# Kernel optimization log

Hardware: AMD Instinct MI355X
Metric: run time of the kernel (lower is better)

## Reference

```python
import jax, jax.numpy as jnp
import numpy as np

VOCAB = 50000
D_EMB = 300
N_BINS = 11
B, LQ, LD = 64, 32, 1024
MU = np.array([1.0, 0.9, 0.7, 0.5, 0.3, 0.1, -0.1, -0.3, -0.5, -0.7, -0.9], dtype=np.float32)
SIGMA = np.array([1e-3] + [0.1] * 10, dtype=np.float32)


def setup_inputs() -> dict:
    key = jax.random.key(0)
    ks = jax.random.split(key, 8)
    inputs_q = jax.random.randint(ks[0], (B, LQ), 0, VOCAB, dtype=jnp.int64 if jax.config.jax_enable_x64 else jnp.int32)
    inputs_d = jax.random.randint(ks[1], (B, LD), 0, VOCAB, dtype=jnp.int64 if jax.config.jax_enable_x64 else jnp.int32)
    mask_q = jnp.ones((B, LQ), dtype=jnp.float32)
    mask_d = jnp.ones((B, LD), dtype=jnp.float32)
    word_emb = jax.random.normal(ks[2], (VOCAB, D_EMB), dtype=jnp.float32) * 0.1
    attn_table = jax.random.uniform(ks[3], (VOCAB, 1), dtype=jnp.float32)  # frozen IDF embedding
    idf_w = jax.random.normal(ks[4], (1, 1), dtype=jnp.float32)
    idf_b = jnp.zeros((1,), dtype=jnp.float32)
    dense_w = jax.random.normal(ks[5], (1, N_BINS), dtype=jnp.float32) * 0.1
    dense_b = jnp.zeros((1,), dtype=jnp.float32)
    return {
        'inputs_q': inputs_q, 'inputs_d': inputs_d,
        'mask_q': mask_q, 'mask_d': mask_d,
        'word_emb': word_emb, 'attn_table': attn_table,
        'idf_w': idf_w, 'idf_b': idf_b,
        'dense_w': dense_w, 'dense_b': dense_b,
    }


def _l2_normalize(x, eps=1e-12):
    # matches F.normalize(x, 2, dim=-1): x / max(||x||, eps)
    n = jnp.sqrt(jnp.sum(x * x, axis=-1, keepdims=True))
    return x / jnp.maximum(n, eps)


def reference(inputs_q, inputs_d, mask_q, mask_d, word_emb, attn_table,
              idf_w, idf_b, dense_w, dense_b):
    mu = jnp.asarray(MU)        # [K]
    sigma = jnp.asarray(SIGMA)  # [K]
    # idf attention on query tokens: Linear(1,1) on frozen embedding lookup
    attn_q = attn_table[inputs_q] * idf_w[0, 0] + idf_b[0]          # [B,Lq,1]
    q_embed = _l2_normalize(word_emb[inputs_q])                      # [B,Lq,E]
    d_embed = _l2_normalize(word_emb[inputs_d])                      # [B,Ld,E]
    sim = jnp.einsum('bqe,bde->bqd', q_embed, d_embed)               # [B,Lq,Ld]
    # RBF soft-histogram over n_bins kernels, doc tokens masked
    rbf = jnp.exp(-((sim[..., None] - mu) ** 2) / (sigma ** 2) / 2)  # [B,Lq,Ld,K]
    pooling_sum = jnp.einsum('bqdk,bd->bqk', rbf, mask_d)            # [B,Lq,K]
    wq = mask_q[..., None] * attn_q                                   # [B,Lq,1]
    log_pool = jnp.log(jnp.clip(pooling_sum, 1e-10)) * wq * 0.01     # [B,Lq,K]
    log_pooling_sum = jnp.sum(log_pool, axis=1)                      # [B,K]
    out = jnp.tanh(log_pooling_sum @ dense_w.T + dense_b)            # [B,1]
    return out[:, 0]                                                 # [B]
```

## Files before the change

### kernel.cpp

```cpp
#include <hip/hip_runtime.h>
#include <math.h>

#define VOCAB  50000
#define D_EMB  300
#define NBINS  11
#define BATCH  64
#define LQ     32
#define LD     1024
#define DTILE  64
#define NDT    (LD / DTILE)
#define NSTEP  10
#define FRAG_SHORTS (NSTEP * 512)

typedef __attribute__((ext_vector_type(8))) short short8;
typedef __attribute__((ext_vector_type(4))) float floatx4;

__constant__ float c_mu[NBINS]  = {1.0f, 0.9f, 0.7f, 0.5f, 0.3f, 0.1f,
                                   -0.1f, -0.3f, -0.5f, -0.7f, -0.9f};
__constant__ float c_is2[NBINS] = {500000.0f, 50.f, 50.f, 50.f, 50.f, 50.f,
                                   50.f, 50.f, 50.f, 50.f, 50.f};

static __device__ __forceinline__ unsigned short f32_bf16(float f) {
  unsigned u = __float_as_uint(f);
  u += 0x7FFFu + ((u >> 16) & 1u);
  return (unsigned short)(u >> 16);
}
static __device__ __forceinline__ float bf16_f32(unsigned short h) {
  return __uint_as_float(((unsigned)h) << 16);
}

static __device__ __forceinline__ float stage_rows(
    const float* __restrict__ emb_row,
    short* __restrict__ region, int khi, int lane)
{
  const float4* emb4 = (const float4*)emb_row;
  float p = 0.f;
#pragma unroll
  for (int s = 0; s < NSTEP; ++s) {
    const int k0 = 32 * s + 8 * khi;
    float4 fa = make_float4(0.f, 0.f, 0.f, 0.f);
    float4 fb = make_float4(0.f, 0.f, 0.f, 0.f);
    if (k0 < D_EMB)     fa = emb4[k0 >> 2];
    if (k0 + 4 < D_EMB) fb = emb4[(k0 >> 2) + 1];
    unsigned short h[8];
    h[0] = f32_bf16(fa.x); h[1] = f32_bf16(fa.y);
    h[2] = f32_bf16(fa.z); h[3] = f32_bf16(fa.w);
    h[4] = f32_bf16(fb.x); h[5] = f32_bf16(fb.y);
    h[6] = f32_bf16(fb.z); h[7] = f32_bf16(fb.w);
    short8 v;
#pragma unroll
    for (int j = 0; j < 8; ++j) {
      const float x = bf16_f32(h[j]);
      p += x * x;
      v[j] = (short)h[j];
    }
    *(short8*)(region + s * 512 + lane * 8) = v;
  }
  return p;
}

__global__ __launch_bounds__(256) void knrm_expand(
    const int* __restrict__ inputs_q, const int* __restrict__ inputs_d,
    const float* __restrict__ word_emb, short* __restrict__ afrag,
    short* __restrict__ dfrag, float* __restrict__ invq,
    float* __restrict__ invd)
{
  const int b    = blockIdx.y;
  const int i    = blockIdx.x * 4 + (threadIdx.x >> 6);
  const int lane = threadIdx.x & 63;
  const int khi  = lane >> 4, rl = lane & 15;
  if (i >= 66) return;

  int tok; short* dst;
  if (i < 2) {
    tok = inputs_q[b * LQ + i * 16 + rl];
    dst = afrag + (size_t)(b * 2 + i) * FRAG_SHORTS;
  } else {
    const int g = i - 2;
    tok = inputs_d[b * LD + g * 16 + rl];
    dst = dfrag + (size_t)(b * 64 + g) * FRAG_SHORTS;
  }
  float p = stage_rows(word_emb + (size_t)tok * D_EMB, dst, khi, lane);
  p += __shfl_xor(p, 16); p += __shfl_xor(p, 32);
  if (lane < 16) {
    const float inv = 1.f / fmaxf(sqrtf(p), 1e-12f);
    if (i < 2) invq[b * LQ + i * 16 + lane] = inv;
    else       invd[b * LD + (i - 2) * 16 + lane] = inv;
  }
}

__global__ __launch_bounds__(256) void knrm_main(
    const float* __restrict__ mask_d, const short* __restrict__ afrag,
    const short* __restrict__ dfrag, const float* __restrict__ invq,
    const float* __restrict__ invd, float* __restrict__ partial)
{
  const int b    = blockIdx.y;
  const int dt   = blockIdx.x;
  const int tid  = threadIdx.x;
  const int wid  = tid >> 6;
  const int lane = tid & 63;
  const int khi  = lane >> 4;
  const int rl   = lane & 15;
  const int qt   = wid >> 1;
  const int dp   = wid & 1;

  __shared__ float red[4][16][NBINS];

  const short8* arow = (const short8*)(afrag + (size_t)(b * 2 + qt) * FRAG_SHORTS);
  const short8* b0r  = (const short8*)(dfrag + (size_t)(b * 64 + dt * 4 + 2 * dp) * FRAG_SHORTS);
  const short8* b1r  = b0r + FRAG_SHORTS / 8;

  floatx4 acc0 = {0.f, 0.f, 0.f, 0.f};
  floatx4 acc1 = {0.f, 0.f, 0.f, 0.f};
#pragma unroll
  for (int s = 0; s < NSTEP; ++s) {
    const short8 a  = arow[s * 64 + lane];
    const short8 b0 = b0r [s * 64 + lane];
    const short8 b1 = b1r [s * 64 + lane];
    acc0 = __builtin_amdgcn_mfma_f32_16x16x32_bf16(a, b0, acc0, 0, 0, 0);
    acc1 = __builtin_amdgcn_mfma_f32_16x16x32_bf16(a, b1, acc1, 0, 0, 0);
  }

  const int dbase = b * LD + dt * DTILE;
  const float iq_own = invq[b * LQ + 16 * qt + rl];
  float iq[4];
#pragma unroll
  for (int r = 0; r < 4; ++r) iq[r] = __shfl(iq_own, 4 * khi + r);
  const float id0 = invd[dbase + 32 * dp + rl];
  const float id1 = invd[dbase + 32 * dp + 16 + rl];
  const float md0 = mask_d[dbase + 32 * dp + rl];
  const float md1 = mask_d[dbase + 32 * dp + 16 + rl];

  float ps[4][NBINS];
#pragma unroll
  for (int r = 0; r < 4; ++r) {
    const float s0 = acc0[r] * iq[r] * id0;
    const float s1 = acc1[r] * iq[r] * id1;
#pragma unroll
    for (int k = 0; k < NBINS; ++k) {
      const float d0 = s0 - c_mu[k];
      const float d1 = s1 - c_mu[k];
      ps[r][k] = md0 * __expf(-d0 * d0 * c_is2[k])
               + md1 * __expf(-d1 * d1 * c_is2[k]);
    }
  }

#pragma unroll
  for (int off = 1; off < 16; off <<= 1)
#pragma unroll
    for (int r = 0; r < 4; ++r)
#pragma unroll
      for (int k = 0; k < NBINS; ++k)
        ps[r][k] += __shfl_xor(ps[r][k], off);

  if (rl == 0)
#pragma unroll
    for (int r = 0; r < 4; ++r)
#pragma unroll
      for (int k = 0; k < NBINS; ++k)
        red[wid][4 * khi + r][k] = ps[r][k];
  __syncthreads();

  for (int v = tid; v < LQ * NBINS; v += 256) {
    const int q = v / NBINS, k = v % NBINS;
    const float sv = (q < 16) ? (red[0][q][k] + red[1][q][k])
                              : (red[2][q - 16][k] + red[3][q - 16][k]);
    partial[((size_t)(b * LQ + q) * NBINS + k) * NDT + dt] = sv;
  }
}

__global__ __launch_bounds__(128) void knrm_finalize(
    const float* __restrict__ partial, const int* __restrict__ inputs_q,
    const float* __restrict__ mask_q, const float* __restrict__ attn_table,
    const float* __restrict__ idf_w, const float* __restrict__ idf_b,
    const float* __restrict__ dense_w, const float* __restrict__ dense_b,
    float* __restrict__ out)
{
  const int b   = blockIdx.x;
  const int tid = threadIdx.x;
  __shared__ float pool[LQ][NBINS];
  __shared__ float wq_s[LQ];
  __shared__ float lps[NBINS];

  for (int v = tid; v < LQ * NBINS; v += 128) {
    const int q = v / NBINS, k = v % NBINS;
    const float* p = partial + ((size_t)(b * LQ + q) * NBINS + k) * NDT;
    float s = 0.f;
#pragma unroll
    for (int t = 0; t < NDT; ++t) s += p[t];
    pool[q][k] = logf(fmaxf(s, 1e-10f));
  }
  if (tid < LQ) {
    const int tok = inputs_q[b * LQ + tid];
    wq_s[tid] = mask_q[b * LQ + tid] * (attn_table[tok] * idf_w[0] + idf_b[0]);
  }
  __syncthreads();
  if (tid < NBINS) {
    float s = 0.f;
    for (int q = 0; q < LQ; ++q) s += pool[q][tid] * wq_s[q];
    lps[tid] = 0.01f * s;
  }
  __syncthreads();
  if (tid == 0) {
    float z = dense_b[0];
    for (int k = 0; k < NBINS; ++k) z += lps[k] * dense_w[k];
    out[b] = tanhf(z);
  }
}

extern "C" void kernel_launch(void* const* d_in, const int* in_sizes, int n_in,
                              void* d_out, int out_size, void* d_ws, size_t ws_size,
                              hipStream_t stream) {
  const int*   inputs_q  = (const int*)d_in[0];
  const int*   inputs_d  = (const int*)d_in[1];
  const float* mask_q    = (const float*)d_in[2];
  const float* mask_d    = (const float*)d_in[3];
  const float* word_emb  = (const float*)d_in[4];
  const float* attn_tab  = (const float*)d_in[5];
  const float* idf_w     = (const float*)d_in[6];
  const float* idf_b     = (const float*)d_in[7];
  const float* dense_w   = (const float*)d_in[8];
  const float* dense_b   = (const float*)d_in[9];
  float* out = (float*)d_out;

  char*  ws      = (char*)d_ws;
  float* partial = (float*)ws;
  short* afrag   = (short*)(ws + (2u  << 20));
  short* dfrag   = (short*)(ws + (4u  << 20));
  float* invq    = (float*)(ws + (48u << 20));
  float* invd    = (float*)(ws + (49u << 20));

  dim3 egrid(17, BATCH);
  knrm_expand<<<egrid, 256, 0, stream>>>(inputs_q, inputs_d, word_emb,
                                         afrag, dfrag, invq, invd);
  dim3 grid(NDT, BATCH);
  knrm_main<<<grid, 256, 0, stream>>>(mask_d, afrag, dfrag, invq, invd, partial);
  knrm_finalize<<<BATCH, 128, 0, stream>>>(partial, inputs_q, mask_q, attn_tab,
                                           idf_w, idf_b, dense_w, dense_b, out);
}
```

Before: 146.5 us.

## Fuse embedding gather and bf16 conversion into the MFMA similarity kernel

Merges the expand kernel into the main kernel. Each block gathers its own doc-token embeddings straight into register fragments and stages the query fragments in LDS. This removes the global round trip of bf16 fragments and inverse norms, plus one kernel launch. Each block now covers 128 doc tokens with both query tiles per wave, giving 8 chunks per batch, so the grid shrinks to 512 blocks. The query embeddings are gathered again by every chunk block, and the larger register-resident fragments may lower occupancy.

```diff
diff --git a/kernel.cpp b/kernel.cpp
--- a/kernel.cpp
+++ b/kernel.cpp
@@ -1,15 +1,14 @@
 #include <hip/hip_runtime.h>
 #include <math.h>
 
-#define VOCAB  50000
-#define D_EMB  300
-#define NBINS  11
-#define BATCH  64
-#define LQ     32
-#define LD     1024
-#define DTILE  64
-#define NDT    (LD / DTILE)
-#define NSTEP  10
+#define VOCAB   50000
+#define D_EMB   300
+#define NBINS   11
+#define BATCH   64
+#define LQ      32
+#define LD      1024
+#define NCHUNK  8
+#define NSTEP   10
 #define FRAG_SHORTS (NSTEP * 512)
 
 typedef __attribute__((ext_vector_type(8))) short short8;
@@ -29,9 +28,9 @@
   return __uint_as_float(((unsigned)h) << 16);
 }
 
-static __device__ __forceinline__ float stage_rows(
-    const float* __restrict__ emb_row,
-    short* __restrict__ region, int khi, int lane)
+static __device__ __forceinline__ float gather_convert(
+    const float* __restrict__ emb_row, short8* __restrict__ frag,
+    int khi)
 {
   const float4* emb4 = (const float4*)emb_row;
   float p = 0.f;
@@ -54,118 +53,104 @@
       p += x * x;
       v[j] = (short)h[j];
     }
-    *(short8*)(region + s * 512 + lane * 8) = v;
+    frag[s] = v;
   }
   return p;
 }
 
-__global__ __launch_bounds__(256) void knrm_expand(
+__global__ __launch_bounds__(256, 2) void knrm_fused(
     const int* __restrict__ inputs_q, const int* __restrict__ inputs_d,
-    const float* __restrict__ word_emb, short* __restrict__ afrag,
-    short* __restrict__ dfrag, float* __restrict__ invq,
-    float* __restrict__ invd)
+    const float* __restrict__ mask_d, const float* __restrict__ word_emb,
+    float* __restrict__ partial)
 {
   const int b    = blockIdx.y;
-  const int i    = blockIdx.x * 4 + (threadIdx.x >> 6);
-  const int lane = threadIdx.x & 63;
-  const int khi  = lane >> 4, rl = lane & 15;
-  if (i >= 66) return;
-
-  int tok; short* dst;
-  if (i < 2) {
-    tok = inputs_q[b * LQ + i * 16 + rl];
-    dst = afrag + (size_t)(b * 2 + i) * FRAG_SHORTS;
-  } else {
-    const int g = i - 2;
-    tok = inputs_d[b * LD + g * 16 + rl];
-    dst = dfrag + (size_t)(b * 64 + g) * FRAG_SHORTS;
-  }
-  float p = stage_rows(word_emb + (size_t)tok * D_EMB, dst, khi, lane);
-  p += __shfl_xor(p, 16); p += __shfl_xor(p, 32);
-  if (lane < 16) {
-    const float inv = 1.f / fmaxf(sqrtf(p), 1e-12f);
-    if (i < 2) invq[b * LQ + i * 16 + lane] = inv;
-    else       invd[b * LD + (i - 2) * 16 + lane] = inv;
-  }
-}
-
-__global__ __launch_bounds__(256) void knrm_main(
-    const float* __restrict__ mask_d, const short* __restrict__ afrag,
-    const short* __restrict__ dfrag, const float* __restrict__ invq,
-    const float* __restrict__ invd, float* __restrict__ partial)
-{
-  const int b    = blockIdx.y;
-  const int dt   = blockIdx.x;
+  const int j    = blockIdx.x;
   const int tid  = threadIdx.x;
   const int wid  = tid >> 6;
   const int lane = tid & 63;
   const int khi  = lane >> 4;
   const int rl   = lane & 15;
-  const int qt   = wid >> 1;
-  const int dp   = wid & 1;
-
-  __shared__ float red[4][16][NBINS];
-
-  const short8* arow = (const short8*)(afrag + (size_t)(b * 2 + qt) * FRAG_SHORTS);
-  const short8* b0r  = (const short8*)(dfrag + (size_t)(b * 64 + dt * 4 + 2 * dp) * FRAG_SHORTS);
-  const short8* b1r  = b0r + FRAG_SHORTS / 8;
-
-  floatx4 acc0 = {0.f, 0.f, 0.f, 0.f};
-  floatx4 acc1 = {0.f, 0.f, 0.f, 0.f};
+
+  __shared__ __align__(16) short Alds[2 * FRAG_SHORTS];
+  __shared__ float invq_lds[LQ];
+  __shared__ float red[4][2][16][NBINS];
+
+  const int dbase = b * LD + j * 128 + 32 * wid;
+
+  const int td0 = inputs_d[dbase + rl];
+  const int td1 = inputs_d[dbase + 16 + rl];
+  short8 bf0[NSTEP], bf1[NSTEP];
+  float pb0 = gather_convert(word_emb + (size_t)td0 * D_EMB, bf0, khi);
+  float pb1 = gather_convert(word_emb + (size_t)td1 * D_EMB, bf1, khi);
+  pb0 += __shfl_xor(pb0, 16); pb0 += __shfl_xor(pb0, 32);
+  pb1 += __shfl_xor(pb1, 16); pb1 += __shfl_xor(pb1, 32);
+  const float id0 = 1.f / fmaxf(sqrtf(pb0), 1e-12f);
+  const float id1 = 1.f / fmaxf(sqrtf(pb1), 1e-12f);
+
+  if (wid < 2) {
+    const int tq = inputs_q[b * LQ + 16 * wid + rl];
+    short8 af[NSTEP];
+    float pa = gather_convert(word_emb + (size_t)tq * D_EMB, af, khi);
+    short8* dst = (short8*)(Alds + wid * FRAG_SHORTS);
+#pragma unroll
+    for (int s = 0; s < NSTEP; ++s) dst[s * 64 + lane] = af[s];
+    pa += __shfl_xor(pa, 16); pa += __shfl_xor(pa, 32);
+    if (lane < 16) invq_lds[16 * wid + lane] = 1.f / fmaxf(sqrtf(pa), 1e-12f);
+  }
+  __syncthreads();
+
+  floatx4 acc[2][2] = {{{0.f,0.f,0.f,0.f},{0.f,0.f,0.f,0.f}},
+                       {{0.f,0.f,0.f,0.f},{0.f,0.f,0.f,0.f}}};
 #pragma unroll
   for (int s = 0; s < NSTEP; ++s) {
-    const short8 a  = arow[s * 64 + lane];
-    const short8 b0 = b0r [s * 64 + lane];
-    const short8 b1 = b1r [s * 64 + lane];
-    acc0 = __builtin_amdgcn_mfma_f32_16x16x32_bf16(a, b0, acc0, 0, 0, 0);
-    acc1 = __builtin_amdgcn_mfma_f32_16x16x32_bf16(a, b1, acc1, 0, 0, 0);
-  }
-
-  const int dbase = b * LD + dt * DTILE;
-  const float iq_own = invq[b * LQ + 16 * qt + rl];
-  float iq[4];
-#pragma unroll
-  for (int r = 0; r < 4; ++r) iq[r] = __shfl(iq_own, 4 * khi + r);
-  const float id0 = invd[dbase + 32 * dp + rl];
-  const float id1 = invd[dbase + 32 * dp + 16 + rl];
-  const float md0 = mask_d[dbase + 32 * dp + rl];
-  const float md1 = mask_d[dbase + 32 * dp + 16 + rl];
-
-  float ps[4][NBINS];
-#pragma unroll
-  for (int r = 0; r < 4; ++r) {
-    const float s0 = acc0[r] * iq[r] * id0;
-    const float s1 = acc1[r] * iq[r] * id1;
-#pragma unroll
-    for (int k = 0; k < NBINS; ++k) {
-      const float d0 = s0 - c_mu[k];
-      const float d1 = s1 - c_mu[k];
-      ps[r][k] = md0 * __expf(-d0 * d0 * c_is2[k])
-               + md1 * __expf(-d1 * d1 * c_is2[k]);
+    const short8 a0 = *(const short8*)(Alds + s * 512 + lane * 8);
+    const short8 a1 = *(const short8*)(Alds + FRAG_SHORTS + s * 512 + lane * 8);
+    acc[0][0] = __builtin_amdgcn_mfma_f32_16x16x32_bf16(a0, bf0[s], acc[0][0], 0, 0, 0);
+    acc[0][1] = __builtin_amdgcn_mfma_f32_16x16x32_bf16(a0, bf1[s], acc[0][1], 0, 0, 0);
+    acc[1][0] = __builtin_amdgcn_mfma_f32_16x16x32_bf16(a1, bf0[s], acc[1][0], 0, 0, 0);
+    acc[1][1] = __builtin_amdgcn_mfma_f32_16x16x32_bf16(a1, bf1[s], acc[1][1], 0, 0, 0);
+  }
+
+  const float md0 = mask_d[dbase + rl];
+  const float md1 = mask_d[dbase + 16 + rl];
+#pragma unroll
+  for (int qt = 0; qt < 2; ++qt) {
+    float ps[4][NBINS];
+#pragma unroll
+    for (int r = 0; r < 4; ++r) {
+      const float iq = invq_lds[16 * qt + 4 * khi + r];
+      const float s0 = acc[qt][0][r] * iq * id0;
+      const float s1 = acc[qt][1][r] * iq * id1;
+#pragma unroll
+      for (int k = 0; k < NBINS; ++k) {
+        const float d0 = s0 - c_mu[k];
+        const float d1 = s1 - c_mu[k];
+        ps[r][k] = md0 * __expf(-d0 * d0 * c_is2[k])
+                 + md1 * __expf(-d1 * d1 * c_is2[k]);
+      }
     }
-  }
-
-#pragma unroll
-  for (int off = 1; off < 16; off <<= 1)
-#pragma unroll
-    for (int r = 0; r < 4; ++r)
-#pragma unroll
-      for (int k = 0; k < NBINS; ++k)
-        ps[r][k] += __shfl_xor(ps[r][k], off);
-
-  if (rl == 0)
-#pragma unroll
-    for (int r = 0; r < 4; ++r)
-#pragma unroll
-      for (int k = 0; k < NBINS; ++k)
-        red[wid][4 * khi + r][k] = ps[r][k];
+#pragma unroll
+    for (int off = 1; off < 16; off <<= 1)
+#pragma unroll
+      for (int r = 0; r < 4; ++r)
+#pragma unroll
+        for (int k = 0; k < NBINS; ++k)
+          ps[r][k] += __shfl_xor(ps[r][k], off);
+    if (rl == 0)
+#pragma unroll
+      for (int r = 0; r < 4; ++r)
+#pragma unroll
+        for (int k = 0; k < NBINS; ++k)
+          red[wid][qt][4 * khi + r][k] = ps[r][k];
+  }
   __syncthreads();
 
   for (int v = tid; v < LQ * NBINS; v += 256) {
     const int q = v / NBINS, k = v % NBINS;
-    const float sv = (q < 16) ? (red[0][q][k] + red[1][q][k])
-                              : (red[2][q - 16][k] + red[3][q - 16][k]);
-    partial[((size_t)(b * LQ + q) * NBINS + k) * NDT + dt] = sv;
+    const int qt = q >> 4, qr = q & 15;
+    const float sv = red[0][qt][qr][k] + red[1][qt][qr][k]
+                   + red[2][qt][qr][k] + red[3][qt][qr][k];
+    partial[((size_t)(b * LQ + q) * NBINS + k) * NCHUNK + j] = sv;
   }
 }
 
@@ -184,10 +169,10 @@
 
   for (int v = tid; v < LQ * NBINS; v += 128) {
     const int q = v / NBINS, k = v % NBINS;
-    const float* p = partial + ((size_t)(b * LQ + q) * NBINS + k) * NDT;
+    const float* p = partial + ((size_t)(b * LQ + q) * NBINS + k) * NCHUNK;
     float s = 0.f;
 #pragma unroll
-    for (int t = 0; t < NDT; ++t) s += p[t];
+    for (int t = 0; t < NCHUNK; ++t) s += p[t];
     pool[q][k] = logf(fmaxf(s, 1e-10f));
   }
   if (tid < LQ) {
@@ -221,20 +206,11 @@
   const float* idf_b     = (const float*)d_in[7];
   const float* dense_w   = (const float*)d_in[8];
   const float* dense_b   = (const float*)d_in[9];
-  float* out = (float*)d_out;
-
-  char*  ws      = (char*)d_ws;
-  float* partial = (float*)ws;
-  short* afrag   = (short*)(ws + (2u  << 20));
-  short* dfrag   = (short*)(ws + (4u  << 20));
-  float* invq    = (float*)(ws + (48u << 20));
-  float* invd    = (float*)(ws + (49u << 20));
-
-  dim3 egrid(17, BATCH);
-  knrm_expand<<<egrid, 256, 0, stream>>>(inputs_q, inputs_d, word_emb,
-                                         afrag, dfrag, invq, invd);
-  dim3 grid(NDT, BATCH);
-  knrm_main<<<grid, 256, 0, stream>>>(mask_d, afrag, dfrag, invq, invd, partial);
+  float* out     = (float*)d_out;
+  float* partial = (float*)d_ws;
+
+  dim3 grid(NCHUNK, BATCH);
+  knrm_fused<<<grid, 256, 0, stream>>>(inputs_q, inputs_d, mask_d, word_emb, partial);
   knrm_finalize<<<BATCH, 128, 0, stream>>>(partial, inputs_q, mask_q, attn_tab,
                                            idf_w, idf_b, dense_w, dense_b, out);
 }
```

Result: faster. 141.9 us (-3.1%).
